# Kernel tuning notes

Hardware: AMD Instinct MI355X
Metric: run time of the kernel (lower is better)

## Reference

```python
import jax, jax.numpy as jnp
import numpy as np


def setup_inputs() -> dict:
    key = jax.random.key(0)
    k1, k2 = jax.random.split(key)
    pred = jax.random.normal(k1, (4, 4096, 3), dtype=jnp.float32)
    gt = jax.random.normal(k2, (4, 4096, 3), dtype=jnp.float32)
    return {"pred": pred, "gt": gt}


def reference(pred, gt):
    # Chamfer distance with L1 (Manhattan) point-to-point distance.
    # pred: [B, N, 3], gt: [B, M, 3]
    # d[b, n, m] = sum_c |pred[b,n,c] - gt[b,m,c]|
    d = jnp.abs(pred[:, :, None, :] - gt[:, None, :, :]).sum(-1)  # [B, N, M]
    cham_x = d.min(axis=2).mean(axis=1)  # nearest gt for each pred point, [B]
    cham_y = d.min(axis=1).mean(axis=1)  # nearest pred for each gt point, [B]
    # point_reduction='mean' per direction, batch_reduction='mean' (pytorch3d default)
    return jnp.mean(cham_x + cham_y)
```

## Files before the change

### kernel.cpp

```cpp
#include <hip/hip_runtime.h>
#include <cfloat>


constexpr int TPB = 256;
constexpr int PTS = 4;
constexpr int NC  = TPB * PTS;
constexpr int MC  = 128;
constexpr int NMC = 4096 / MC;

__global__ __launch_bounds__(TPB, 4) void chamfer_partial_kernel(
    const float* __restrict__ pred, const float* __restrict__ gt,
    float* __restrict__ partial, float* __restrict__ out,
    int B, int N, int M) {
    const int dir = blockIdx.z;
    const int b   = blockIdx.y;
    const float* q = dir ? gt   : pred;
    const float* t = dir ? pred : gt;
    const int Nq   = dir ? M : N;
    const int Nt   = dir ? N : M;
    const int nchunks = Nq / NC;
    const int nc = blockIdx.x % nchunks;
    const int mc = blockIdx.x / nchunks;

    if (blockIdx.x == 0 && blockIdx.y == 0 && blockIdx.z == 0 &&
        threadIdx.x == 0) out[0] = 0.0f;

    __shared__ float tlds[MC * 3];

    const float* tbase = t + ((size_t)b * Nt + (size_t)mc * MC) * 3;
    for (int i = threadIdx.x; i < MC * 3; i += TPB) tlds[i] = tbase[i];
    __syncthreads();

    const float* qb = q + (size_t)b * Nq * 3;
    float px[PTS], py[PTS], pz[PTS], mn[PTS];
    int n[PTS];
#pragma unroll
    for (int i = 0; i < PTS; ++i) {
        n[i] = nc * NC + threadIdx.x + i * TPB;
        px[i] = qb[n[i] * 3 + 0];
        py[i] = qb[n[i] * 3 + 1];
        pz[i] = qb[n[i] * 3 + 2];
        mn[i] = FLT_MAX;
    }

#pragma unroll 4
    for (int jg = 0; jg < MC / 4; ++jg) {
        const float4 A  = ((const float4*)tlds)[3 * jg + 0];
        const float4 Bv = ((const float4*)tlds)[3 * jg + 1];
        const float4 Cv = ((const float4*)tlds)[3 * jg + 2];
#pragma unroll
        for (int i = 0; i < PTS; ++i) {
            float d0 = fabsf(px[i] - A.x)  + fabsf(py[i] - A.y)  + fabsf(pz[i] - A.z);
            float d1 = fabsf(px[i] - A.w)  + fabsf(py[i] - Bv.x) + fabsf(pz[i] - Bv.y);
            float d2 = fabsf(px[i] - Bv.z) + fabsf(py[i] - Bv.w) + fabsf(pz[i] - Cv.x);
            float d3 = fabsf(px[i] - Cv.y) + fabsf(py[i] - Cv.z) + fabsf(pz[i] - Cv.w);
            mn[i] = fminf(mn[i], fminf(fminf(d0, d1), fminf(d2, d3)));
        }
    }

    float* outp = partial + (((size_t)mc * 2 + dir) * B + b) * N;
#pragma unroll
    for (int i = 0; i < PTS; ++i) outp[n[i]] = mn[i];
}

__global__ __launch_bounds__(256) void chamfer_reduce_kernel(
    const float* __restrict__ partial, float* __restrict__ out,
    int Q, float inv) {
    const int qidx = blockIdx.x * 256 + threadIdx.x;
    float mn = FLT_MAX;
#pragma unroll
    for (int mc = 0; mc < NMC; ++mc)
        mn = fminf(mn, partial[(size_t)mc * Q + qidx]);
    float v = mn * inv;

    for (int off = 32; off > 0; off >>= 1) v += __shfl_down(v, off, 64);
    __shared__ float red[4];
    const int lane = threadIdx.x & 63, w = threadIdx.x >> 6;
    if (lane == 0) red[w] = v;
    __syncthreads();
    if (threadIdx.x == 0)
        atomicAdd(out, red[0] + red[1] + red[2] + red[3]);
}

extern "C" void kernel_launch(void* const* d_in, const int* in_sizes, int n_in,
                              void* d_out, int out_size, void* d_ws, size_t ws_size,
                              hipStream_t stream) {
    const float* pred = (const float*)d_in[0];
    const float* gt   = (const float*)d_in[1];
    float* out = (float*)d_out;

    const int B = 4;
    const int N = in_sizes[0] / (B * 3);
    const int M = in_sizes[1] / (B * 3);

    float* partial = (float*)d_ws;
    const int Q = 2 * B * N;

    dim3 grid((N / NC) * (M / MC), B, 2);
    chamfer_partial_kernel<<<grid, TPB, 0, stream>>>(pred, gt, partial, out,
                                                     B, N, M);

    chamfer_reduce_kernel<<<Q / 256, 256, 0, stream>>>(
        partial, out, Q, 1.0f / (float)(B * N));
}
```

Before: 78.05 us.

## Compute L1 distances in packed fp16 with interleaved half2 LDS layout

Converts query and target coordinates to fp16 and repacks the shared target tile so pairs of points sit together per coordinate. The distance and min loop then uses packed half2 subtract, abs, add and min, handling two targets per instruction. This is meant to roughly halve the VALU work in the inner loop and halve the LDS footprint. It gives up accuracy: fp16 rounding of coordinates and distances loosens the final tolerance.

```diff
diff --git a/kernel.cpp b/kernel.cpp
--- a/kernel.cpp
+++ b/kernel.cpp
@@ -1,12 +1,24 @@
 #include <hip/hip_runtime.h>
 #include <cfloat>
 
+
+typedef _Float16 half2v __attribute__((ext_vector_type(2)));
 
 constexpr int TPB = 256;
 constexpr int PTS = 4;
 constexpr int NC  = TPB * PTS;
 constexpr int MC  = 128;
 constexpr int NMC = 4096 / MC;
+
+__device__ __forceinline__ half2v h2min(half2v a, half2v b) {
+    return __builtin_elementwise_min(a, b);
+}
+__device__ __forceinline__ half2v h2abs(half2v a) {
+    return __builtin_elementwise_abs(a);
+}
+__device__ __forceinline__ half2v bits_to_h2(unsigned u) {
+    union { unsigned u; half2v h; } c; c.u = u; return c.h;
+}
 
 __global__ __launch_bounds__(TPB, 4) void chamfer_partial_kernel(
     const float* __restrict__ pred, const float* __restrict__ gt,
@@ -25,42 +37,58 @@
     if (blockIdx.x == 0 && blockIdx.y == 0 && blockIdx.z == 0 &&
         threadIdx.x == 0) out[0] = 0.0f;
 
-    __shared__ float tlds[MC * 3];
+    __shared__ _Float16 tlds[MC * 3];
 
     const float* tbase = t + ((size_t)b * Nt + (size_t)mc * MC) * 3;
-    for (int i = threadIdx.x; i < MC * 3; i += TPB) tlds[i] = tbase[i];
+    for (int i = threadIdx.x; i < MC * 3; i += TPB) {
+        int m = i / 3, c = i % 3;
+        tlds[6 * (m >> 1) + 2 * c + (m & 1)] = (_Float16)tbase[i];
+    }
     __syncthreads();
 
     const float* qb = q + (size_t)b * Nq * 3;
-    float px[PTS], py[PTS], pz[PTS], mn[PTS];
+    half2v px2[PTS], py2[PTS], pz2[PTS], mn2[PTS];
     int n[PTS];
 #pragma unroll
     for (int i = 0; i < PTS; ++i) {
         n[i] = nc * NC + threadIdx.x + i * TPB;
-        px[i] = qb[n[i] * 3 + 0];
-        py[i] = qb[n[i] * 3 + 1];
-        pz[i] = qb[n[i] * 3 + 2];
-        mn[i] = FLT_MAX;
+        _Float16 x = (_Float16)qb[n[i] * 3 + 0];
+        _Float16 y = (_Float16)qb[n[i] * 3 + 1];
+        _Float16 z = (_Float16)qb[n[i] * 3 + 2];
+        px2[i] = (half2v){x, x};
+        py2[i] = (half2v){y, y};
+        pz2[i] = (half2v){z, z};
+        mn2[i] = (half2v){(_Float16)65504.0f, (_Float16)65504.0f};
     }
 
 #pragma unroll 4
-    for (int jg = 0; jg < MC / 4; ++jg) {
-        const float4 A  = ((const float4*)tlds)[3 * jg + 0];
-        const float4 Bv = ((const float4*)tlds)[3 * jg + 1];
-        const float4 Cv = ((const float4*)tlds)[3 * jg + 2];
+    for (int jg = 0; jg < MC / 8; ++jg) {
+        const uint4 A = ((const uint4*)tlds)[3 * jg + 0];
+        const uint4 Bv = ((const uint4*)tlds)[3 * jg + 1];
+        const uint4 Cv = ((const uint4*)tlds)[3 * jg + 2];
+        const half2v gx[4] = {bits_to_h2(A.x),  bits_to_h2(A.w),
+                              bits_to_h2(Bv.z), bits_to_h2(Cv.y)};
+        const half2v gy[4] = {bits_to_h2(A.y),  bits_to_h2(Bv.x),
+                              bits_to_h2(Bv.w), bits_to_h2(Cv.z)};
+        const half2v gz[4] = {bits_to_h2(A.z),  bits_to_h2(Bv.y),
+                              bits_to_h2(Cv.x), bits_to_h2(Cv.w)};
 #pragma unroll
-        for (int i = 0; i < PTS; ++i) {
-            float d0 = fabsf(px[i] - A.x)  + fabsf(py[i] - A.y)  + fabsf(pz[i] - A.z);
-            float d1 = fabsf(px[i] - A.w)  + fabsf(py[i] - Bv.x) + fabsf(pz[i] - Bv.y);
-            float d2 = fabsf(px[i] - Bv.z) + fabsf(py[i] - Bv.w) + fabsf(pz[i] - Cv.x);
-            float d3 = fabsf(px[i] - Cv.y) + fabsf(py[i] - Cv.z) + fabsf(pz[i] - Cv.w);
-            mn[i] = fminf(mn[i], fminf(fminf(d0, d1), fminf(d2, d3)));
+        for (int tp = 0; tp < 4; ++tp) {
+#pragma unroll
+            for (int i = 0; i < PTS; ++i) {
+                half2v d = h2abs(px2[i] - gx[tp]) + h2abs(py2[i] - gy[tp])
+                         + h2abs(pz2[i] - gz[tp]);
+                mn2[i] = h2min(mn2[i], d);
+            }
         }
     }
 
     float* outp = partial + (((size_t)mc * 2 + dir) * B + b) * N;
 #pragma unroll
-    for (int i = 0; i < PTS; ++i) outp[n[i]] = mn[i];
+    for (int i = 0; i < PTS; ++i) {
+        float lo = (float)mn2[i].x, hi = (float)mn2[i].y;
+        outp[n[i]] = fminf(lo, hi);
+    }
 }
 
 __global__ __launch_bounds__(256) void chamfer_reduce_kernel(
```

Result: no change. 76.67 us (-1.8%).
